# Kernel tuning notes

Hardware: AMD Instinct MI355X
Metric: run time of the kernel (lower is better)

The kernel has to match this reference:

```python
import jax, jax.numpy as jnp
import numpy as np

B, N, D, KG, L = 4, 256, 256, 128, 2
EPS = 1e-5


def setup_inputs() -> dict:
    key = jax.random.key(0)
    ks = jax.random.split(key, 8)
    s = 0.05  # weight init scale
    return {
        "node_feats": jax.random.normal(ks[0], (B, N, D), dtype=jnp.float32),
        "kg_relation_embeddings": jax.random.normal(ks[1], (B, N, N, KG), dtype=jnp.float32),
        "kg_adjacency": jax.random.randint(ks[2], (B, N, N), 0, 2, dtype=jnp.int32),
        # kg_proj: Linear(kg_embed_dim -> node_dim)
        "W_kg": (jax.random.normal(ks[3], (KG, D), dtype=jnp.float32) * s),
        "b_kg": jnp.zeros((D,), dtype=jnp.float32),
        # per-layer MLP: Linear(3D -> D), ReLU, Linear(D -> D); stacked over L layers
        "W1": (jax.random.normal(ks[4], (L, 3 * D, D), dtype=jnp.float32) * s),
        "b1": jnp.zeros((L, D), dtype=jnp.float32),
        "W2": (jax.random.normal(ks[5], (L, D, D), dtype=jnp.float32) * s),
        "b2": jnp.zeros((L, D), dtype=jnp.float32),
        # shared LayerNorm(node_dim)
        "gamma": jnp.ones((D,), dtype=jnp.float32),
        "beta": jnp.zeros((D,), dtype=jnp.float32),
    }


def _layer_norm(x, gamma, beta):
    mu = x.mean(-1, keepdims=True)
    var = ((x - mu) ** 2).mean(-1, keepdims=True)
    return (x - mu) * jax.lax.rsqrt(var + EPS) * gamma + beta


def reference(node_feats, kg_relation_embeddings, kg_adjacency,
              W_kg, b_kg, W1, b1, W2, b2, gamma, beta):
    d = node_feats.shape[-1]
    n_layers = W1.shape[0]
    # kg_proj applied to relation embeddings (same every layer; dropout is eval-mode identity)
    rel_proj = kg_relation_embeddings @ W_kg + b_kg            # (B,N,N,D)
    adj = kg_adjacency[..., None].astype(node_feats.dtype)     # (B,N,N,1)
    h = node_feats
    for l in range(n_layers):
        # split first Linear over the concat [hi, hj, rel_proj] -> avoids building (B,N,N,3D)
        Wa, Wb, Wc = W1[l, :d], W1[l, d:2 * d], W1[l, 2 * d:]
        a = h @ Wa                                             # (B,N,D) contribution of hi
        b = h @ Wb                                             # (B,N,D) contribution of hj
        c = jnp.einsum('bijk,kd->bijd', rel_proj, Wc)          # (B,N,N,D)
        pre = a[:, :, None, :] + b[:, None, :, :] + c + b1[l]  # (B,N,N,D)
        m = jax.nn.relu(pre) @ W2[l] + b2[l]                   # (B,N,N,D)
        msg = (m * adj).sum(axis=2)                            # (B,N,D) sum over source nodes j
        h = _layer_norm(h + msg, gamma, beta)
    return h
```

## Files before the change

### kernel.cpp

```cpp
#include <hip/hip_runtime.h>
#include <hip/hip_bf16.h>

#define B_ 4
#define N_ 256
#define D_ 256
#define KG_ 128
#define EPS_ 1e-5f

typedef __bf16 bf16x8 __attribute__((ext_vector_type(8)));
typedef __bf16 bf16x4 __attribute__((ext_vector_type(4)));
typedef float  f32x4v __attribute__((ext_vector_type(4)));

__device__ __forceinline__ void gload16(const void* g, void* l) {
    __builtin_amdgcn_global_load_lds(
        (const __attribute__((address_space(1))) uint32_t*)g,
        (__attribute__((address_space(3))) uint32_t*)l, 16, 0, 0);
}

__global__ __launch_bounds__(256) void s1_kernel(
    const float* __restrict__ Wkg, const float* __restrict__ W1l,
    const float* __restrict__ bkg, const float* __restrict__ b1l,
    __bf16* __restrict__ WkcT, float* __restrict__ biastot)
{
    const int d = threadIdx.x;
    if (blockIdx.x == KG_) {
        float acc = 0.f;
        for (int k = 0; k < D_; ++k)
            acc += bkg[k] * W1l[(2 * D_ + k) * D_ + d];
        biastot[d] = acc + b1l[d];
        return;
    }
    const int g = blockIdx.x;
    float acc = 0.f;
    for (int k = 0; k < D_; ++k)
        acc += Wkg[g * D_ + k] * W1l[(2 * D_ + k) * D_ + d];
    WkcT[d * KG_ + g] = (__bf16)acc;
}

__global__ __launch_bounds__(256) void s2_kernel(
    const float* __restrict__ hin, const float* __restrict__ W1l,
    const float* __restrict__ biastot,
    float* __restrict__ apb, __bf16* __restrict__ bbout)
{
    __shared__ float hT[D_][4];
    const int tid = threadIdx.x;
    const int R = blockIdx.x * 4;
    {
        const int r = tid & 3, c4 = (tid >> 2) << 2;
        const float4 v = *(const float4*)(hin + (R + r) * D_ + c4);
        hT[c4 + 0][r] = v.x; hT[c4 + 1][r] = v.y;
        hT[c4 + 2][r] = v.z; hT[c4 + 3][r] = v.w;
    }
    __syncthreads();
    float aa[4] = {0.f, 0.f, 0.f, 0.f};
    float ab[4] = {0.f, 0.f, 0.f, 0.f};
#pragma unroll 4
    for (int e = 0; e < D_; ++e) {
        const float wa = W1l[e * D_ + tid];
        const float wb = W1l[(D_ + e) * D_ + tid];
        const float4 hv = *(const float4*)&hT[e][0];
        aa[0] += hv.x * wa; aa[1] += hv.y * wa; aa[2] += hv.z * wa; aa[3] += hv.w * wa;
        ab[0] += hv.x * wb; ab[1] += hv.y * wb; ab[2] += hv.z * wb; ab[3] += hv.w * wb;
    }
    const float bt = biastot[tid];
#pragma unroll
    for (int r = 0; r < 4; ++r) {
        apb[(R + r) * D_ + tid]    = aa[r] + bt;
        bbout[(R + r) * D_ + tid]  = (__bf16)ab[r];
    }
}

__global__ __launch_bounds__(256, 2) void big_kernel(
    const float* __restrict__ rel, const int* __restrict__ adj,
    const __bf16* __restrict__ WkcT, const float* __restrict__ apb,
    const __bf16* __restrict__ bb, const float* __restrict__ W2l,
    const float* __restrict__ b2l, const float* __restrict__ hin,
    const float* __restrict__ gmm, const float* __restrict__ bta,
    float* __restrict__ hout)
{
    __shared__ __align__(16) __bf16 Et[64 * KG_];
    __shared__ __align__(16) __bf16 Bt[64 * D_];
    __shared__ float adjL[N_];
    __shared__ float rL[D_];
    __shared__ float red[8];
    __shared__ float sdeg;

    const int tid = threadIdx.x;
    const int lane = tid & 63;
    const int w = tid >> 6;
    const int l15 = lane & 15;
    const int lg = lane >> 4;
    const int bi = blockIdx.x;
    const int dw = w * 64;

    const float*  Ebase  = rel + (size_t)bi * N_ * KG_;
    const __bf16* bbBase = bb + (size_t)(bi >> 8) * N_ * D_;

    bf16x8 wf[4][4];
#pragma unroll
    for (int nb = 0; nb < 4; ++nb)
#pragma unroll
        for (int kk = 0; kk < 4; ++kk)
            wf[nb][kk] = *(const bf16x8*)(WkcT + (dw + nb * 16 + l15) * KG_ + kk * 32 + lg * 8);

    f32x4v apbv[4];
#pragma unroll
    for (int nb = 0; nb < 4; ++nb)
        apbv[nb] = *(const f32x4v*)(apb + bi * D_ + dw + nb * 16 + lg * 4);

    adjL[tid] = (float)adj[bi * N_ + tid];

    float racc[4][4] = {};

    for (int jq = 0; jq < 4; ++jq) {
        {
            const char* Gb = (const char*)(bbBase + jq * 64 * D_);
            char* ldsw = (char*)Bt + (tid & 192) * 16;
#pragma unroll
            for (int i = 0; i < 8; ++i) {
                const int u = tid + i * 256;
                const int gu = (u & ~31) | ((u & 31) ^ ((u >> 5) & 7));
                gload16(Gb + gu * 16, ldsw + i * 4096);
            }
        }
        {
#pragma unroll
            for (int rep = 0; rep < 4; ++rep) {
                const int v = tid + rep * 256;
                const int row = v >> 4;
                const int k0 = (v & 15) * 8;
                const float* s = Ebase + (jq * 64 + row) * KG_ + k0;
                const f32x4v fa = *(const f32x4v*)s;
                const f32x4v fb = *(const f32x4v*)(s + 4);
                bf16x8 v8;
                v8[0] = (__bf16)fa[0]; v8[1] = (__bf16)fa[1];
                v8[2] = (__bf16)fa[2]; v8[3] = (__bf16)fa[3];
                v8[4] = (__bf16)fb[0]; v8[5] = (__bf16)fb[1];
                v8[6] = (__bf16)fb[2]; v8[7] = (__bf16)fb[3];
                const int off = (row * 256 + k0 * 2) ^ ((row & 7) << 4);
                *(bf16x8*)((char*)Et + off) = v8;
            }
        }
        __syncthreads();

#pragma unroll
        for (int jj = 0; jj < 4; ++jj) {
            const int row = jj * 16 + l15;
            bf16x8 af[4];
#pragma unroll
            for (int kk = 0; kk < 4; ++kk) {
                const int off = (row * 256 + kk * 64 + lg * 16) ^ ((row & 7) << 4);
                af[kk] = *(const bf16x8*)((const char*)Et + off);
            }
            f32x4v acc[4];
#pragma unroll
            for (int nb = 0; nb < 4; ++nb) acc[nb] = (f32x4v){0.f, 0.f, 0.f, 0.f};
#pragma unroll
            for (int kk = 0; kk < 4; ++kk)
#pragma unroll
                for (int nb = 0; nb < 4; ++nb)
                    acc[nb] = __builtin_amdgcn_mfma_f32_16x16x32_bf16(wf[nb][kk], af[kk], acc[nb], 0, 0, 0);

            const float adjj = adjL[jq * 64 + row];
#pragma unroll
            for (int nb = 0; nb < 4; ++nb) {
                const int dbyte = w * 128 + nb * 32 + lg * 8;
                const int su = (dbyte >> 4) ^ (row & 7);
                const bf16x4 bv = *(const bf16x4*)((const char*)Bt + row * 512 + su * 16 + (dbyte & 15));
#pragma unroll
                for (int q = 0; q < 4; ++q) {
                    float t = acc[nb][q] + apbv[nb][q] + (float)bv[q];
                    t = fmaxf(t, 0.f);
                    racc[nb][q] += t * adjj;
                }
            }
        }
        __syncthreads();
    }

#pragma unroll
    for (int nb = 0; nb < 4; ++nb) {
        float v0 = racc[nb][0], v1 = racc[nb][1], v2 = racc[nb][2], v3 = racc[nb][3];
#pragma unroll
        for (int off = 1; off <= 8; off <<= 1) {
            v0 += __shfl_xor(v0, off, 64);
            v1 += __shfl_xor(v1, off, 64);
            v2 += __shfl_xor(v2, off, 64);
            v3 += __shfl_xor(v3, off, 64);
        }
        if (l15 == 0) {
            float4 o; o.x = v0; o.y = v1; o.z = v2; o.w = v3;
            *(float4*)&rL[dw + nb * 16 + lg * 4] = o;
        }
    }
    if (w == 0) {
        float s = adjL[lane] + adjL[lane + 64] + adjL[lane + 128] + adjL[lane + 192];
#pragma unroll
        for (int off = 32; off >= 1; off >>= 1) s += __shfl_xor(s, off, 64);
        if (lane == 0) sdeg = s;
    }
    __syncthreads();

    const int d = tid;
    float m0 = 0.f, m1 = 0.f, m2 = 0.f, m3 = 0.f;
    for (int e = 0; e < D_; e += 4) {
        const float4 rv = *(const float4*)&rL[e];
        m0 += rv.x * W2l[(e + 0) * D_ + d];
        m1 += rv.y * W2l[(e + 1) * D_ + d];
        m2 += rv.z * W2l[(e + 2) * D_ + d];
        m3 += rv.w * W2l[(e + 3) * D_ + d];
    }
    const float t = hin[bi * D_ + d] + (m0 + m1) + (m2 + m3) + sdeg * b2l[d];

    float s = t, sq = t * t;
#pragma unroll
    for (int off = 32; off >= 1; off >>= 1) {
        s  += __shfl_xor(s, off, 64);
        sq += __shfl_xor(sq, off, 64);
    }
    if (lane == 0) { red[w] = s; red[4 + w] = sq; }
    __syncthreads();
    const float S  = red[0] + red[1] + red[2] + red[3];
    const float SQ = red[4] + red[5] + red[6] + red[7];
    const float mu = S * (1.f / D_);
    const float var = SQ * (1.f / D_) - mu * mu;
    const float rstd = rsqrtf(var + EPS_);
    hout[bi * D_ + d] = (t - mu) * rstd * gmm[d] + bta[d];
}

extern "C" void kernel_launch(void* const* d_in, const int* in_sizes, int n_in,
                              void* d_out, int out_size, void* d_ws, size_t ws_size,
                              hipStream_t stream)
{
    const float* node  = (const float*)d_in[0];
    const float* rel   = (const float*)d_in[1];
    const int*   adj   = (const int*)d_in[2];
    const float* Wkg   = (const float*)d_in[3];
    const float* bkg   = (const float*)d_in[4];
    const float* W1    = (const float*)d_in[5];
    const float* b1    = (const float*)d_in[6];
    const float* W2    = (const float*)d_in[7];
    const float* b2    = (const float*)d_in[8];
    const float* gamma = (const float*)d_in[9];
    const float* beta  = (const float*)d_in[10];
    float* out = (float*)d_out;

    char* ws = (char*)d_ws;
    float*  h1    = (float*)(ws);
    float*  apb   = (float*)(ws + (1 << 20));
    __bf16* bbuf  = (__bf16*)(ws + (2 << 20));
    float*  bias  = (float*)(ws + (3 << 20));
    __bf16* WkcT  = (__bf16*)(ws + (3 << 20) + 4096);

    for (int l = 0; l < 2; ++l) {
        const float* W1l = W1 + (size_t)l * 3 * D_ * D_;
        const float* hin = (l == 0) ? node : h1;
        float* hout = (l == 1) ? out : h1;

        s1_kernel<<<KG_ + 1, 256, 0, stream>>>(Wkg, W1l, bkg, b1 + l * D_, WkcT, bias);
        s2_kernel<<<(B_ * N_) / 4, 256, 0, stream>>>(hin, W1l, bias, apb, bbuf);
        big_kernel<<<B_ * N_, 256, 0, stream>>>(rel, adj, WkcT, apb, bbuf,
                                                W2 + (size_t)l * D_ * D_, b2 + l * D_,
                                                hin, gamma, beta, hout);
    }
}
```

Measured before the change: 178.4 us.

## Load relation rows straight into registers with double buffering instead of LDS staging

The LDS staging of the relation-embedding tile and the hj-contribution tile is removed. Each wave now loads its 16-row slice of fp32 embeddings directly into registers, converts it to bf16 MFMA operands, and double-buffers the loads across 16 row-blocks so the next block's loads overlap the current block's MFMAs. The bb values are read straight from global memory per row. This drops the per-chunk __syncthreads and the LDS traffic. In exchange, each of the 4 waves redundantly loads the same E rows, since they all cover the same j rows for different d columns. Register pressure also rises with 16 float4 buffers on top of the 16 bf16x8 weight fragments.

```diff
diff --git a/kernel.cpp b/kernel.cpp
--- a/kernel.cpp
+++ b/kernel.cpp
@@ -10,12 +10,6 @@
 typedef __bf16 bf16x8 __attribute__((ext_vector_type(8)));
 typedef __bf16 bf16x4 __attribute__((ext_vector_type(4)));
 typedef float  f32x4v __attribute__((ext_vector_type(4)));
-
-__device__ __forceinline__ void gload16(const void* g, void* l) {
-    __builtin_amdgcn_global_load_lds(
-        (const __attribute__((address_space(1))) uint32_t*)g,
-        (__attribute__((address_space(3))) uint32_t*)l, 16, 0, 0);
-}
 
 __global__ __launch_bounds__(256) void s1_kernel(
     const float* __restrict__ Wkg, const float* __restrict__ W1l,
@@ -78,8 +72,6 @@
     const float* __restrict__ gmm, const float* __restrict__ bta,
     float* __restrict__ hout)
 {
-    __shared__ __align__(16) __bf16 Et[64 * KG_];
-    __shared__ __align__(16) __bf16 Bt[64 * D_];
     __shared__ float adjL[N_];
     __shared__ float rL[D_];
     __shared__ float red[8];
@@ -109,73 +101,64 @@
         apbv[nb] = *(const f32x4v*)(apb + bi * D_ + dw + nb * 16 + lg * 4);
 
     adjL[tid] = (float)adj[bi * N_ + tid];
+    __syncthreads();
 
     float racc[4][4] = {};
 
-    for (int jq = 0; jq < 4; ++jq) {
-        {
-            const char* Gb = (const char*)(bbBase + jq * 64 * D_);
-            char* ldsw = (char*)Bt + (tid & 192) * 16;
-#pragma unroll
-            for (int i = 0; i < 8; ++i) {
-                const int u = tid + i * 256;
-                const int gu = (u & ~31) | ((u & 31) ^ ((u >> 5) & 7));
-                gload16(Gb + gu * 16, ldsw + i * 4096);
+    const float* esrc = Ebase + l15 * KG_ + lg * 8;
+
+    auto eload = [&](int jj, f32x4v* e) {
+        const float* s = esrc + jj * 16 * KG_;
+#pragma unroll
+        for (int kk = 0; kk < 4; ++kk) {
+            e[2 * kk]     = *(const f32x4v*)(s + kk * 32);
+            e[2 * kk + 1] = *(const f32x4v*)(s + kk * 32 + 4);
+        }
+    };
+
+    auto docompute = [&](int jj, const f32x4v* e) {
+        bf16x8 af[4];
+#pragma unroll
+        for (int kk = 0; kk < 4; ++kk) {
+            const f32x4v fa = e[2 * kk];
+            const f32x4v fb = e[2 * kk + 1];
+            bf16x8 v;
+            v[0] = (__bf16)fa[0]; v[1] = (__bf16)fa[1]; v[2] = (__bf16)fa[2]; v[3] = (__bf16)fa[3];
+            v[4] = (__bf16)fb[0]; v[5] = (__bf16)fb[1]; v[6] = (__bf16)fb[2]; v[7] = (__bf16)fb[3];
+            af[kk] = v;
+        }
+        f32x4v acc[4];
+#pragma unroll
+        for (int nb = 0; nb < 4; ++nb) acc[nb] = (f32x4v){0.f, 0.f, 0.f, 0.f};
+#pragma unroll
+        for (int kk = 0; kk < 4; ++kk)
+#pragma unroll
+            for (int nb = 0; nb < 4; ++nb)
+                acc[nb] = __builtin_amdgcn_mfma_f32_16x16x32_bf16(wf[nb][kk], af[kk], acc[nb], 0, 0, 0);
+
+        const int row = jj * 16 + l15;
+        const float adjj = adjL[row];
+        const __bf16* brow = bbBase + row * D_ + dw + lg * 4;
+#pragma unroll
+        for (int nb = 0; nb < 4; ++nb) {
+            const bf16x4 bv = *(const bf16x4*)(brow + nb * 16);
+#pragma unroll
+            for (int q = 0; q < 4; ++q) {
+                float t = acc[nb][q] + apbv[nb][q] + (float)bv[q];
+                t = fmaxf(t, 0.f);
+                racc[nb][q] += t * adjj;
             }
         }
-        {
-#pragma unroll
-            for (int rep = 0; rep < 4; ++rep) {
-                const int v = tid + rep * 256;
-                const int row = v >> 4;
-                const int k0 = (v & 15) * 8;
-                const float* s = Ebase + (jq * 64 + row) * KG_ + k0;
-                const f32x4v fa = *(const f32x4v*)s;
-                const f32x4v fb = *(const f32x4v*)(s + 4);
-                bf16x8 v8;
-                v8[0] = (__bf16)fa[0]; v8[1] = (__bf16)fa[1];
-                v8[2] = (__bf16)fa[2]; v8[3] = (__bf16)fa[3];
-                v8[4] = (__bf16)fb[0]; v8[5] = (__bf16)fb[1];
-                v8[6] = (__bf16)fb[2]; v8[7] = (__bf16)fb[3];
-                const int off = (row * 256 + k0 * 2) ^ ((row & 7) << 4);
-                *(bf16x8*)((char*)Et + off) = v8;
-            }
-        }
-        __syncthreads();
-
-#pragma unroll
-        for (int jj = 0; jj < 4; ++jj) {
-            const int row = jj * 16 + l15;
-            bf16x8 af[4];
-#pragma unroll
-            for (int kk = 0; kk < 4; ++kk) {
-                const int off = (row * 256 + kk * 64 + lg * 16) ^ ((row & 7) << 4);
-                af[kk] = *(const bf16x8*)((const char*)Et + off);
-            }
-            f32x4v acc[4];
-#pragma unroll
-            for (int nb = 0; nb < 4; ++nb) acc[nb] = (f32x4v){0.f, 0.f, 0.f, 0.f};
-#pragma unroll
-            for (int kk = 0; kk < 4; ++kk)
-#pragma unroll
-                for (int nb = 0; nb < 4; ++nb)
-                    acc[nb] = __builtin_amdgcn_mfma_f32_16x16x32_bf16(wf[nb][kk], af[kk], acc[nb], 0, 0, 0);
-
-            const float adjj = adjL[jq * 64 + row];
-#pragma unroll
-            for (int nb = 0; nb < 4; ++nb) {
-                const int dbyte = w * 128 + nb * 32 + lg * 8;
-                const int su = (dbyte >> 4) ^ (row & 7);
-                const bf16x4 bv = *(const bf16x4*)((const char*)Bt + row * 512 + su * 16 + (dbyte & 15));
-#pragma unroll
-                for (int q = 0; q < 4; ++q) {
-                    float t = acc[nb][q] + apbv[nb][q] + (float)bv[q];
-                    t = fmaxf(t, 0.f);
-                    racc[nb][q] += t * adjj;
-                }
-            }
-        }
-        __syncthreads();
+    };
+
+    f32x4v eA[8], eB[8];
+    eload(0, eA);
+#pragma unroll
+    for (int jj = 0; jj < 16; jj += 2) {
+        if (jj + 1 < 16) eload(jj + 1, eB);
+        docompute(jj, eA);
+        if (jj + 2 < 16) eload(jj + 2, eA);
+        if (jj + 1 < 16) docompute(jj + 1, eB);
     }
 
 #pragma unroll
```

Measured after the change: 597.8 us. 235% more time.

## Cache bf16 relation embeddings in workspace for layer 2 and load whole tile once

Applied to the files above, without the earlier changes.

Layer 1 converts the fp32 relation embeddings to bf16 and writes them to a workspace buffer. Layer 2 then reads that half-size copy with async global-to-LDS loads instead of re-reading the fp32 tensor. Each block now stages all 256 rows of its relation tile into LDS in one pass and drops the per-quarter loop and its barriers. The bb tile is read directly from global memory instead of through LDS. The larger 64KB LDS footprint and the removed occupancy hint may lower occupancy and serialise load against compute, and the new path only runs if the workspace is large enough.

```diff
diff --git a/kernel.cpp b/kernel.cpp
--- a/kernel.cpp
+++ b/kernel.cpp
@@ -70,16 +70,17 @@
     }
 }
 
-__global__ __launch_bounds__(256, 2) void big_kernel(
-    const float* __restrict__ rel, const int* __restrict__ adj,
+template<int FROMB>
+__global__ __launch_bounds__(256) void big_kernel(
+    const float* __restrict__ rel, __bf16* __restrict__ relb,
+    const int* __restrict__ adj,
     const __bf16* __restrict__ WkcT, const float* __restrict__ apb,
     const __bf16* __restrict__ bb, const float* __restrict__ W2l,
     const float* __restrict__ b2l, const float* __restrict__ hin,
     const float* __restrict__ gmm, const float* __restrict__ bta,
     float* __restrict__ hout)
 {
-    __shared__ __align__(16) __bf16 Et[64 * KG_];
-    __shared__ __align__(16) __bf16 Bt[64 * D_];
+    __shared__ __align__(16) __bf16 Et[N_ * KG_];
     __shared__ float adjL[N_];
     __shared__ float rL[D_];
     __shared__ float red[8];
@@ -110,72 +111,69 @@
 
     adjL[tid] = (float)adj[bi * N_ + tid];
 
+    if (FROMB) {
+        const char* Gb = (const char*)(relb + (size_t)bi * N_ * KG_);
+        char* ldsw = (char*)Et + (tid & 192) * 16;
+#pragma unroll
+        for (int i = 0; i < 16; ++i) {
+            const int u = tid + i * 256;
+            const int gu = (u & ~15) | ((u & 15) ^ ((u >> 4) & 7));
+            gload16(Gb + gu * 16, ldsw + i * 4096);
+        }
+    } else {
+        __bf16* relbW = relb ? relb + (size_t)bi * N_ * KG_ : nullptr;
+#pragma unroll
+        for (int rep = 0; rep < 16; ++rep) {
+            const int v = tid + rep * 256;
+            const int row = v >> 4;
+            const int k0 = (v & 15) * 8;
+            const float* s = Ebase + row * KG_ + k0;
+            const f32x4v fa = *(const f32x4v*)s;
+            const f32x4v fb = *(const f32x4v*)(s + 4);
+            bf16x8 v8;
+            v8[0] = (__bf16)fa[0]; v8[1] = (__bf16)fa[1];
+            v8[2] = (__bf16)fa[2]; v8[3] = (__bf16)fa[3];
+            v8[4] = (__bf16)fb[0]; v8[5] = (__bf16)fb[1];
+            v8[6] = (__bf16)fb[2]; v8[7] = (__bf16)fb[3];
+            const int off = (row * 256 + k0 * 2) ^ ((row & 7) << 4);
+            *(bf16x8*)((char*)Et + off) = v8;
+            if (relbW) *(bf16x8*)(relbW + v * 8) = v8;
+        }
+    }
+    __syncthreads();
+
     float racc[4][4] = {};
 
-    for (int jq = 0; jq < 4; ++jq) {
-        {
-            const char* Gb = (const char*)(bbBase + jq * 64 * D_);
-            char* ldsw = (char*)Bt + (tid & 192) * 16;
-#pragma unroll
-            for (int i = 0; i < 8; ++i) {
-                const int u = tid + i * 256;
-                const int gu = (u & ~31) | ((u & 31) ^ ((u >> 5) & 7));
-                gload16(Gb + gu * 16, ldsw + i * 4096);
+#pragma unroll 4
+    for (int jj = 0; jj < 16; ++jj) {
+        const int row = jj * 16 + l15;
+        bf16x8 af[4];
+#pragma unroll
+        for (int kk = 0; kk < 4; ++kk) {
+            const int off = (row * 256 + kk * 64 + lg * 16) ^ ((row & 7) << 4);
+            af[kk] = *(const bf16x8*)((const char*)Et + off);
+        }
+        f32x4v acc[4];
+#pragma unroll
+        for (int nb = 0; nb < 4; ++nb) acc[nb] = (f32x4v){0.f, 0.f, 0.f, 0.f};
+#pragma unroll
+        for (int kk = 0; kk < 4; ++kk)
+#pragma unroll
+            for (int nb = 0; nb < 4; ++nb)
+                acc[nb] = __builtin_amdgcn_mfma_f32_16x16x32_bf16(wf[nb][kk], af[kk], acc[nb], 0, 0, 0);
+
+        const float adjj = adjL[row];
+        const __bf16* brow = bbBase + row * D_ + dw + lg * 4;
+#pragma unroll
+        for (int nb = 0; nb < 4; ++nb) {
+            const bf16x4 bv = *(const bf16x4*)(brow + nb * 16);
+#pragma unroll
+            for (int q = 0; q < 4; ++q) {
+                float t = acc[nb][q] + apbv[nb][q] + (float)bv[q];
+                t = fmaxf(t, 0.f);
+                racc[nb][q] += t * adjj;
             }
         }
-        {
-#pragma unroll
-            for (int rep = 0; rep < 4; ++rep) {
-                const int v = tid + rep * 256;
-                const int row = v >> 4;
-                const int k0 = (v & 15) * 8;
-                const float* s = Ebase + (jq * 64 + row) * KG_ + k0;
-                const f32x4v fa = *(const f32x4v*)s;
-                const f32x4v fb = *(const f32x4v*)(s + 4);
-                bf16x8 v8;
-                v8[0] = (__bf16)fa[0]; v8[1] = (__bf16)fa[1];
-                v8[2] = (__bf16)fa[2]; v8[3] = (__bf16)fa[3];
-                v8[4] = (__bf16)fb[0]; v8[5] = (__bf16)fb[1];
-                v8[6] = (__bf16)fb[2]; v8[7] = (__bf16)fb[3];
-                const int off = (row * 256 + k0 * 2) ^ ((row & 7) << 4);
-                *(bf16x8*)((char*)Et + off) = v8;
-            }
-        }
-        __syncthreads();
-
-#pragma unroll
-        for (int jj = 0; jj < 4; ++jj) {
-            const int row = jj * 16 + l15;
-            bf16x8 af[4];
-#pragma unroll
-            for (int kk = 0; kk < 4; ++kk) {
-                const int off = (row * 256 + kk * 64 + lg * 16) ^ ((row & 7) << 4);
-                af[kk] = *(const bf16x8*)((const char*)Et + off);
-            }
-            f32x4v acc[4];
-#pragma unroll
-            for (int nb = 0; nb < 4; ++nb) acc[nb] = (f32x4v){0.f, 0.f, 0.f, 0.f};
-#pragma unroll
-            for (int kk = 0; kk < 4; ++kk)
-#pragma unroll
-                for (int nb = 0; nb < 4; ++nb)
-                    acc[nb] = __builtin_amdgcn_mfma_f32_16x16x32_bf16(wf[nb][kk], af[kk], acc[nb], 0, 0, 0);
-
-            const float adjj = adjL[jq * 64 + row];
-#pragma unroll
-            for (int nb = 0; nb < 4; ++nb) {
-                const int dbyte = w * 128 + nb * 32 + lg * 8;
-                const int su = (dbyte >> 4) ^ (row & 7);
-                const bf16x4 bv = *(const bf16x4*)((const char*)Bt + row * 512 + su * 16 + (dbyte & 15));
-#pragma unroll
-                for (int q = 0; q < 4; ++q) {
-                    float t = acc[nb][q] + apbv[nb][q] + (float)bv[q];
-                    t = fmaxf(t, 0.f);
-                    racc[nb][q] += t * adjj;
-                }
-            }
-        }
-        __syncthreads();
     }
 
 #pragma unroll
@@ -203,6 +201,7 @@
 
     const int d = tid;
     float m0 = 0.f, m1 = 0.f, m2 = 0.f, m3 = 0.f;
+#pragma unroll 8
     for (int e = 0; e < D_; e += 4) {
         const float4 rv = *(const float4*)&rL[e];
         m0 += rv.x * W2l[(e + 0) * D_ + d];
@@ -251,6 +250,11 @@
     __bf16* bbuf  = (__bf16*)(ws + (2 << 20));
     float*  bias  = (float*)(ws + (3 << 20));
     __bf16* WkcT  = (__bf16*)(ws + (3 << 20) + 4096);
+    __bf16* relb  = (__bf16*)(ws + (8 << 20));
+
+    const size_t relElems = (size_t)B_ * N_ * N_ * KG_;
+    const bool useBF = ws_size >= ((size_t)(8 << 20) + relElems * 2);
+    __bf16* relbArg = useBF ? relb : nullptr;
 
     for (int l = 0; l < 2; ++l) {
         const float* W1l = W1 + (size_t)l * 3 * D_ * D_;
@@ -259,8 +263,13 @@
 
         s1_kernel<<<KG_ + 1, 256, 0, stream>>>(Wkg, W1l, bkg, b1 + l * D_, WkcT, bias);
         s2_kernel<<<(B_ * N_) / 4, 256, 0, stream>>>(hin, W1l, bias, apb, bbuf);
-        big_kernel<<<B_ * N_, 256, 0, stream>>>(rel, adj, WkcT, apb, bbuf,
-                                                W2 + (size_t)l * D_ * D_, b2 + l * D_,
-                                                hin, gamma, beta, hout);
-    }
-}
+        if (l == 0 || !useBF)
+            big_kernel<0><<<B_ * N_, 256, 0, stream>>>(rel, relbArg, adj, WkcT, apb, bbuf,
+                                                       W2 + (size_t)l * D_ * D_, b2 + l * D_,
+                                                       hin, gamma, beta, hout);
+        else
+            big_kernel<1><<<B_ * N_, 256, 0, stream>>>(rel, relbArg, adj, WkcT, apb, bbuf,
+                                                       W2 + (size_t)l * D_ * D_, b2 + l * D_,
+                                                       hin, gamma, beta, hout);
+    }
+}
```

Measured after the change: 208.5 us. 16.9% more time.
